# Kernel tuning notes

Measured on AMD Instinct MI355X. Metric: run time of the kernel, lower is better.

Reference implementation:

```python
import jax, jax.numpy as jnp
import numpy as np

EPS = 1e-5
N_HEADS = 4
N_GROUPS = 32


def group_norm(x, gamma, beta, num_groups):
    # x: (B, C, H, W)
    B, C, H, W = x.shape
    xg = x.reshape(B, num_groups, (C // num_groups) * H * W)
    mean = xg.mean(axis=2, keepdims=True)
    var = xg.var(axis=2, keepdims=True)
    xn = ((xg - mean) * jax.lax.rsqrt(var + EPS)).reshape(B, C, H, W)
    return xn * gamma[None, :, None, None] + beta[None, :, None, None]


def conv1x1(x, W, b=None):
    # 1x1 conv == channel-mixing matmul: (O,C) x (B,C,H,W) -> (B,O,H,W)
    y = jnp.einsum('oc,bchw->bohw', W, x)
    if b is not None:
        y = y + b[None, :, None, None]
    return y


def setup_inputs() -> dict:
    key = jax.random.key(0)
    ks = jax.random.split(key, 8)
    B, Cq, Cc, H, W = 2, 128, 128, 64, 64
    x = jax.random.normal(ks[0], (B, Cq, H, W), dtype=jnp.float32)
    context = jax.random.normal(ks[1], (B, Cc, H, W), dtype=jnp.float32)
    sq = Cq ** -0.5
    sc = Cc ** -0.5
    return {
        'x': x,
        'context': context,
        'gq': jnp.ones((Cq,), jnp.float32),
        'bq': jnp.zeros((Cq,), jnp.float32),
        'gctx': jnp.ones((Cc,), jnp.float32),
        'bctx': jnp.zeros((Cc,), jnp.float32),
        'Wq': jax.random.normal(ks[2], (Cq, Cq), jnp.float32) * sq,
        'Wk': jax.random.normal(ks[3], (Cq, Cc), jnp.float32) * sc,
        'Wv': jax.random.normal(ks[4], (Cq, Cc), jnp.float32) * sc,
        'Wout': jax.random.normal(ks[5], (Cq, Cq), jnp.float32) * 0.02,
        'bout': jnp.zeros((Cq,), jnp.float32),
        'alpha': jnp.asarray(1.0, jnp.float32),
    }


def reference(x, context, gq, bq, gctx, bctx, Wq, Wk, Wv, Wout, bout, alpha):
    B, C, H, W = x.shape
    hd = C // N_HEADS
    # QKV projections (GroupNorm + 1x1 conv); note v uses raw context (no norm)
    q = conv1x1(group_norm(x, gq, bq, N_GROUPS), Wq)
    k = conv1x1(group_norm(context, gctx, bctx, N_GROUPS), Wk)
    v = conv1x1(context, Wv)
    q = q.reshape(B, N_HEADS, hd, H * W)
    k = k.reshape(B, N_HEADS, hd, H * W)
    v = v.reshape(B, N_HEADS, hd, H * W)
    scale = jnp.asarray(hd ** 0.5, x.dtype)
    attn = jnp.einsum('bncd,bnce->bnde', q, k) / scale  # (B, nH, HW, HW)
    attn = jax.nn.softmax(attn, axis=-1)
    out = jnp.einsum('bnde,bnce->bncd', attn, v).reshape(B, C, H, W)
    return x + alpha * conv1x1(out, Wout, bout)
```

## Files before the change

kernel.cpp:

```cpp
#include <hip/hip_runtime.h>
#include <hip/hip_bf16.h>
#include <math.h>

#define L 4096
#define C 128
#define NH 4
#define HD 32
#define KS 4
#define EPSV 1e-5f

typedef short bf16x8 __attribute__((ext_vector_type(8)));
typedef float f32x4 __attribute__((ext_vector_type(4)));

static __device__ __forceinline__ unsigned pack2bf(float a, float b) {
    __hip_bfloat162 h = __float22bfloat162_rn(make_float2(a, b));
    unsigned u; __builtin_memcpy(&u, &h, 4); return u;
}
static __device__ __forceinline__ float bf_lo(unsigned u) {
    unsigned v = u << 16; float f; __builtin_memcpy(&f, &v, 4); return f;
}
static __device__ __forceinline__ float bf_hi(unsigned u) {
    unsigned v = u & 0xffff0000u; float f; __builtin_memcpy(&f, &v, 4); return f;
}
static __device__ __forceinline__ float fast_exp2(float x) {
    float t = fmaf(x, 8388608.f, 1064992212.f);
    int i = (int)t;
    float r; __builtin_memcpy(&r, &i, 4);
    return r;
}

__global__ __launch_bounds__(256) void gn_stats_kernel(
    const float* __restrict__ x, const float* __restrict__ ctx,
    float* __restrict__ stats)
{
    int bid = blockIdx.x;
    int t = threadIdx.x;
    const float* in = (bid < 256) ? x : ctx;
    int idx = bid & 255;
    const float4* p = (const float4*)(in + (size_t)(idx >> 2) * 16384
                                         + (size_t)(idx & 3) * 4096);
    float s = 0.f, s2 = 0.f;
    #pragma unroll
    for (int rr = 0; rr < 4; rr++) {
        float4 v = p[t + rr * 256];
        s  += v.x + v.y + v.z + v.w;
        s2 += v.x*v.x + v.y*v.y + v.z*v.z + v.w*v.w;
    }
    #pragma unroll
    for (int m = 32; m >= 1; m >>= 1) {
        s  += __shfl_xor(s, m);
        s2 += __shfl_xor(s2, m);
    }
    __shared__ float wsum[4][2];
    int w = t >> 6;
    if ((t & 63) == 0) { wsum[w][0] = s; wsum[w][1] = s2; }
    __syncthreads();
    if (t == 0) {
        float S  = wsum[0][0] + wsum[1][0] + wsum[2][0] + wsum[3][0];
        float S2 = wsum[0][1] + wsum[1][1] + wsum[2][1] + wsum[3][1];
        stats[bid * 2]     = S;
        stats[bid * 2 + 1] = S2;
    }
}

__global__ __launch_bounds__(256) void proj_kernel(
    const float* __restrict__ x, const float* __restrict__ ctx,
    const float* __restrict__ gq, const float* __restrict__ bq,
    const float* __restrict__ gctx, const float* __restrict__ bctx,
    const float* __restrict__ stats,
    const float* __restrict__ Wq, const float* __restrict__ Wk,
    const float* __restrict__ Wv,
    unsigned short* __restrict__ Qt, unsigned short* __restrict__ Kt,
    unsigned short* __restrict__ Vsw)
{
    int t = threadIdx.x;
    int w = t >> 6, lane = t & 63, n16 = lane & 15, quad = lane >> 4;
    int dtile = blockIdx.x * 32;
    int b = blockIdx.y, z = blockIdx.z;

    const float* in; const float* Wm; const float* gamma; const float* beta;
    int sel = 1, donorm = 1; float oscale = 1.f;
    if (z == 0)      { in = x;   Wm = Wq; gamma = gq;   beta = bq;   sel = 0;
                       oscale = 0.17677669529663689f * 1.4426950408889634f; }
    else if (z == 1) { in = ctx; Wm = Wk; gamma = gctx; beta = bctx; }
    else             { in = ctx; Wm = Wv; gamma = 0;    beta = 0;    donorm = 0; }

    __shared__ __attribute__((aligned(16))) unsigned short Xs[32 * 136];

    {
        int c0 = (t >> 3) * 4, d4 = (t & 7) * 4;
        const float* inb = in + (size_t)b * (C * L);
        float sc0 = 1.f, sh0 = 0.f;
        float scg[4], shg[4];
        if (donorm) {
            int gl = (sel * 256 + (b * 32 + (c0 >> 2)) * 4) * 2;
            float S  = stats[gl] + stats[gl + 2] + stats[gl + 4] + stats[gl + 6];
            float S2 = stats[gl + 1] + stats[gl + 3] + stats[gl + 5] + stats[gl + 7];
            float mean = S * (1.f / 16384.f);
            float var  = S2 * (1.f / 16384.f) - mean * mean;
            float inv  = rsqrtf(var + EPSV);
            #pragma unroll
            for (int j = 0; j < 4; j++) {
                scg[j] = inv * gamma[c0 + j];
                shg[j] = beta[c0 + j] - mean * scg[j];
            }
        } else {
            #pragma unroll
            for (int j = 0; j < 4; j++) { scg[j] = 1.f; shg[j] = 0.f; }
        }
        (void)sc0; (void)sh0;
        float vv[4][4];
        #pragma unroll
        for (int j = 0; j < 4; j++) {
            float4 v = *(const float4*)(inb + (size_t)(c0 + j) * L + dtile + d4);
            vv[j][0] = v.x * scg[j] + shg[j]; vv[j][1] = v.y * scg[j] + shg[j];
            vv[j][2] = v.z * scg[j] + shg[j]; vv[j][3] = v.w * scg[j] + shg[j];
        }
        #pragma unroll
        for (int i = 0; i < 4; i++) {
            uint2 pk;
            pk.x = pack2bf(vv[0][i], vv[1][i]);
            pk.y = pack2bf(vv[2][i], vv[3][i]);
            *(uint2*)&Xs[(d4 + i) * 136 + c0] = pk;
        }
    }

    bf16x8 wa[2][4];
    #pragma unroll
    for (int os2 = 0; os2 < 2; os2++) {
        const float* wr = Wm + (size_t)(((w + os2 * 4) * 16) + n16) * C + quad * 8;
        #pragma unroll
        for (int kk = 0; kk < 4; kk++) {
            float4 a  = *(const float4*)(wr + kk * 32);
            float4 b2 = *(const float4*)(wr + kk * 32 + 4);
            unsigned u4[4] = { pack2bf(a.x, a.y),  pack2bf(a.z, a.w),
                               pack2bf(b2.x, b2.y), pack2bf(b2.z, b2.w) };
            __builtin_memcpy(&wa[os2][kk], u4, 16);
        }
    }
    __syncthreads();

    f32x4 zero = {0.f, 0.f, 0.f, 0.f};
    f32x4 acc[2][2];
    acc[0][0] = zero; acc[0][1] = zero; acc[1][0] = zero; acc[1][1] = zero;
    #pragma unroll
    for (int kk = 0; kk < 4; kk++) {
        #pragma unroll
        for (int dg = 0; dg < 2; dg++) {
            bf16x8 xb;
            uint4 u = *(const uint4*)&Xs[(dg * 16 + n16) * 136 + kk * 32 + quad * 8];
            __builtin_memcpy(&xb, &u, 16);
            acc[0][dg] = __builtin_amdgcn_mfma_f32_16x16x32_bf16(wa[0][kk], xb, acc[0][dg], 0, 0, 0);
            acc[1][dg] = __builtin_amdgcn_mfma_f32_16x16x32_bf16(wa[1][kk], xb, acc[1][dg], 0, 0, 0);
        }
    }

    #pragma unroll
    for (int os2 = 0; os2 < 2; os2++) {
        int o = ((w + os2 * 4) * 16) + quad * 4;
        int h = o >> 5, c32 = o & 31;
        #pragma unroll
        for (int dg = 0; dg < 2; dg++) {
            int d = dtile + dg * 16 + n16;
            if (z < 2) {
                unsigned short* outp = (z == 0) ? Qt : Kt;
                uint2 pk;
                pk.x = pack2bf(acc[os2][dg][0] * oscale, acc[os2][dg][1] * oscale);
                pk.y = pack2bf(acc[os2][dg][2] * oscale, acc[os2][dg][3] * oscale);
                *(uint2*)(outp + ((size_t)(b * NH + h) * L + d) * HD + c32) = pk;
            } else {
                unsigned short* vb = Vsw + (size_t)(b * NH + h) * (L * HD)
                                   + (size_t)(d >> 3) * 256 + (d & 7);
                #pragma unroll
                for (int r = 0; r < 4; r++) {
                    __hip_bfloat16 hv = __float2bfloat16(acc[os2][dg][r]);
                    unsigned short us; __builtin_memcpy(&us, &hv, 2);
                    vb[(c32 + r) * 8] = us;
                }
            }
        }
    }
}

__global__ __launch_bounds__(256, 4) void flash_kernel(
    const unsigned short* __restrict__ Qt, const unsigned short* __restrict__ Kt,
    const unsigned short* __restrict__ Vsw, unsigned short* __restrict__ Po,
    float* __restrict__ Pl)
{
    __shared__ __attribute__((aligned(16))) unsigned short Ps[4 * 2 * 1152];

    int t = threadIdx.x;
    int w = t >> 6, lane = t & 63;
    int n16 = lane & 15, quad = lane >> 4;
    int bh = blockIdx.x;
    int qbase = blockIdx.y * 128 + w * 32;
    int ks = blockIdx.z;
    size_t hb = (size_t)bh * (L * HD);

    bf16x8 qf[2];
    #pragma unroll
    for (int sp = 0; sp < 2; sp++) {
        uint4 u = *(const uint4*)(Qt + hb + (size_t)(qbase + sp * 16 + n16) * HD + quad * 8);
        __builtin_memcpy(&qf[sp], &u, 16);
    }

    bf16x8 onesf;
    #pragma unroll
    for (int j = 0; j < 8; j++) onesf[j] = (short)0x3F80;

    const unsigned short* kfp = Kt + hb + (size_t)n16 * HD + quad * 8;
    const unsigned short* vfp = Vsw + hb + quad * 256 + n16 * 8;

    int e0 = ks * (L / KS);

    bf16x8 ka[2][4], va[2][4];
    #pragma unroll
    for (int et = 0; et < 4; et++) {
        uint4 u = *(const uint4*)(kfp + (size_t)(e0 + et * 16) * HD);
        __builtin_memcpy(&ka[0][et], &u, 16);
    }
    #pragma unroll
    for (int es = 0; es < 2; es++)
        #pragma unroll
        for (int f = 0; f < 2; f++) {
            uint4 u = *(const uint4*)(vfp + (size_t)(e0 + es * 32) * 32 + f * 128);
            __builtin_memcpy(&va[0][es * 2 + f], &u, 16);
        }

    f32x4 zero = {0.f, 0.f, 0.f, 0.f};
    f32x4 oacc[2][2], lacc[2];
    oacc[0][0] = zero; oacc[0][1] = zero; oacc[1][0] = zero; oacc[1][1] = zero;
    lacc[0] = zero; lacc[1] = zero;

    #pragma unroll 2
    for (int kt = 0; kt < L / KS / 64; kt++) {
        int cur = kt & 1, nxt = cur ^ 1;
        int enxt = e0 + (kt + 1) * 64;
        #pragma unroll
        for (int et = 0; et < 4; et++) {
            uint4 u = *(const uint4*)(kfp + (size_t)(enxt + et * 16) * HD);
            __builtin_memcpy(&ka[nxt][et], &u, 16);
        }
        #pragma unroll
        for (int es = 0; es < 2; es++)
            #pragma unroll
            for (int f = 0; f < 2; f++) {
                uint4 u = *(const uint4*)(vfp + (size_t)(enxt + es * 32) * 32 + f * 128);
                __builtin_memcpy(&va[nxt][es * 2 + f], &u, 16);
            }

        #pragma unroll
        for (int sp = 0; sp < 2; sp++) {
            f32x4 s[4];
            #pragma unroll
            for (int et = 0; et < 4; et++)
                s[et] = __builtin_amdgcn_mfma_f32_16x16x32_bf16(ka[cur][et], qf[sp], zero, 0, 0, 0);
            unsigned short* pw = Ps + ((w * 2 + sp) * 1152) + n16 * 72;
            #pragma unroll
            for (int et = 0; et < 4; et++) {
                uint2 pk;
                pk.x = pack2bf(fast_exp2(s[et][0]), fast_exp2(s[et][1]));
                pk.y = pack2bf(fast_exp2(s[et][2]), fast_exp2(s[et][3]));
                *(uint2*)(pw + et * 16 + quad * 4) = pk;
            }
        }

        #pragma unroll
        for (int sp = 0; sp < 2; sp++) {
            unsigned short* pw = Ps + ((w * 2 + sp) * 1152) + n16 * 72;
            #pragma unroll
            for (int es = 0; es < 2; es++) {
                bf16x8 pf;
                uint4 u = *(const uint4*)(pw + es * 32 + quad * 8);
                __builtin_memcpy(&pf, &u, 16);
                oacc[sp][0] = __builtin_amdgcn_mfma_f32_16x16x32_bf16(va[cur][es * 2 + 0], pf, oacc[sp][0], 0, 0, 0);
                oacc[sp][1] = __builtin_amdgcn_mfma_f32_16x16x32_bf16(va[cur][es * 2 + 1], pf, oacc[sp][1], 0, 0, 0);
                lacc[sp]    = __builtin_amdgcn_mfma_f32_16x16x32_bf16(onesf, pf, lacc[sp], 0, 0, 0);
            }
        }
    }

    #pragma unroll
    for (int sp = 0; sp < 2; sp++) {
        int dq = qbase + sp * 16 + n16;
        unsigned short* po = Po + ((size_t)(bh * KS + ks) * L + dq) * 32;
        uint2 pk0, pk1;
        pk0.x = pack2bf(oacc[sp][0][0], oacc[sp][0][1]);
        pk0.y = pack2bf(oacc[sp][0][2], oacc[sp][0][3]);
        pk1.x = pack2bf(oacc[sp][1][0], oacc[sp][1][1]);
        pk1.y = pack2bf(oacc[sp][1][2], oacc[sp][1][3]);
        *(uint2*)(po + quad * 4)      = pk0;
        *(uint2*)(po + 16 + quad * 4) = pk1;
        if (quad == 0)
            Pl[(size_t)(bh * KS + ks) * L + dq] = lacc[sp][0];
    }
}

__global__ __launch_bounds__(256) void final_kernel(
    const unsigned short* __restrict__ Po, const float* __restrict__ Pl,
    const float* __restrict__ x, const float* __restrict__ Wout,
    const float* __restrict__ bout, const float* __restrict__ alpha,
    float* __restrict__ out)
{
    int t = threadIdx.x;
    int w = t >> 6, lane = t & 63, n16 = lane & 15, quad = lane >> 4;
    int dtile = blockIdx.x * 16;
    int b = blockIdx.y;

    __shared__ __attribute__((aligned(16))) float Ot[128 * 20];
    unsigned short* Xs = (unsigned short*)Ot;

    {
        int d_l = t >> 4, c0 = (t & 15) * 8;
        int dq = dtile + d_l;
        int bh = b * NH + (c0 >> 5);
        int c32 = c0 & 31;
        float l = 0.f;
        float o8[8] = {0.f, 0.f, 0.f, 0.f, 0.f, 0.f, 0.f, 0.f};
        #pragma unroll
        for (int ks = 0; ks < KS; ks++) {
            size_t base = (size_t)(bh * KS + ks) * L + dq;
            l += Pl[base];
            uint4 u = *(const uint4*)(Po + base * 32 + c32);
            o8[0] += bf_lo(u.x); o8[1] += bf_hi(u.x);
            o8[2] += bf_lo(u.y); o8[3] += bf_hi(u.y);
            o8[4] += bf_lo(u.z); o8[5] += bf_hi(u.z);
            o8[6] += bf_lo(u.w); o8[7] += bf_hi(u.w);
        }
        float rl = 1.f / l;
        uint4 pk;
        pk.x = pack2bf(o8[0] * rl, o8[1] * rl);
        pk.y = pack2bf(o8[2] * rl, o8[3] * rl);
        pk.z = pack2bf(o8[4] * rl, o8[5] * rl);
        pk.w = pack2bf(o8[6] * rl, o8[7] * rl);
        *(uint4*)&Xs[d_l * 136 + c0] = pk;
    }

    bf16x8 wa[2][4];
    #pragma unroll
    for (int os2 = 0; os2 < 2; os2++) {
        const float* wr = Wout + (size_t)(((w + os2 * 4) * 16) + n16) * C + quad * 8;
        #pragma unroll
        for (int kk = 0; kk < 4; kk++) {
            float4 a  = *(const float4*)(wr + kk * 32);
            float4 b2 = *(const float4*)(wr + kk * 32 + 4);
            unsigned u4[4] = { pack2bf(a.x, a.y),  pack2bf(a.z, a.w),
                               pack2bf(b2.x, b2.y), pack2bf(b2.z, b2.w) };
            __builtin_memcpy(&wa[os2][kk], u4, 16);
        }
    }
    __syncthreads();

    f32x4 zero = {0.f, 0.f, 0.f, 0.f};
    f32x4 acc[2];
    acc[0] = zero; acc[1] = zero;
    #pragma unroll
    for (int kk = 0; kk < 4; kk++) {
        bf16x8 xb;
        uint4 u = *(const uint4*)&Xs[n16 * 136 + kk * 32 + quad * 8];
        __builtin_memcpy(&xb, &u, 16);
        acc[0] = __builtin_amdgcn_mfma_f32_16x16x32_bf16(wa[0][kk], xb, acc[0], 0, 0, 0);
        acc[1] = __builtin_amdgcn_mfma_f32_16x16x32_bf16(wa[1][kk], xb, acc[1], 0, 0, 0);
    }
    __syncthreads();

    #pragma unroll
    for (int os2 = 0; os2 < 2; os2++) {
        int o = ((w + os2 * 4) * 16) + quad * 4;
        #pragma unroll
        for (int r = 0; r < 4; r++)
            Ot[(o + r) * 20 + n16] = acc[os2][r];
    }
    __syncthreads();

    float al = alpha[0];
    int o = t >> 1, dh = (t & 1) * 8;
    float bo = bout[o];
    const float* xb2 = x + ((size_t)b * C + o) * L + dtile + dh;
    float* ob = out + ((size_t)b * C + o) * L + dtile + dh;
    #pragma unroll
    for (int jj = 0; jj < 2; jj++) {
        float4 a  = *(const float4*)&Ot[o * 20 + dh + jj * 4];
        float4 xv = *(const float4*)(xb2 + jj * 4);
        float4 r;
        r.x = xv.x + al * (a.x + bo);
        r.y = xv.y + al * (a.y + bo);
        r.z = xv.z + al * (a.z + bo);
        r.w = xv.w + al * (a.w + bo);
        *(float4*)(ob + jj * 4) = r;
    }
}

extern "C" void kernel_launch(void* const* d_in, const int* in_sizes, int n_in,
                              void* d_out, int out_size, void* d_ws, size_t ws_size,
                              hipStream_t stream) {
    const float* x     = (const float*)d_in[0];
    const float* ctx   = (const float*)d_in[1];
    const float* gq    = (const float*)d_in[2];
    const float* bq    = (const float*)d_in[3];
    const float* gctx  = (const float*)d_in[4];
    const float* bctx  = (const float*)d_in[5];
    const float* Wq    = (const float*)d_in[6];
    const float* Wk    = (const float*)d_in[7];
    const float* Wv    = (const float*)d_in[8];
    const float* Wout  = (const float*)d_in[9];
    const float* bout  = (const float*)d_in[10];
    const float* alpha = (const float*)d_in[11];
    float* out = (float*)d_out;

    char* ws = (char*)d_ws;
    unsigned short* Qt  = (unsigned short*)(ws);
    unsigned short* Kt  = (unsigned short*)(ws + 2097152);
    unsigned short* Vsw = (unsigned short*)(ws + 4194304);
    unsigned short* Po  = (unsigned short*)(ws + 6291456);
    float*          Pl  = (float*)(ws + 14680064);
    float*          stats = (float*)(ws + 15204352);

    gn_stats_kernel<<<512, 256, 0, stream>>>(x, ctx, stats);
    proj_kernel<<<dim3(128, 2, 3), 256, 0, stream>>>(x, ctx, gq, bq, gctx, bctx,
                                                     stats, Wq, Wk, Wv, Qt, Kt, Vsw);
    flash_kernel<<<dim3(8, 32, KS), 256, 0, stream>>>(Qt, Kt, Vsw, Po, Pl);
    final_kernel<<<dim3(256, 2), 256, 0, stream>>>(Po, Pl, x, Wout, bout, alpha, out);
}
```

Baseline: 127.8 us.

## Keep softmax probabilities in registers via f16 MFMA, removing the LDS round-trip

The flash kernel no longer writes exp'd scores to shared memory and reads them back for the PV product. The S accumulator layout from the 16x16x32 MFMA is fed directly as the B operand of 16x16x16 f16 MFMAs. This needs V re-laid out in f16 with a 4-wide swizzle, written by the projection kernel. The cost is twice as many PV/row-sum MFMAs at half depth, V loads that are no longer double-buffered across iterations, and f16 range for V and P, with round-toward-zero packing of P.

Result: slower. 134.0 us (+4.9%).

```diff
diff --git a/kernel.cpp b/kernel.cpp
--- a/kernel.cpp
+++ b/kernel.cpp
@@ -11,6 +11,7 @@
 
 typedef short bf16x8 __attribute__((ext_vector_type(8)));
 typedef float f32x4 __attribute__((ext_vector_type(4)));
+typedef _Float16 f16x4 __attribute__((ext_vector_type(4)));
 
 static __device__ __forceinline__ unsigned pack2bf(float a, float b) {
     __hip_bfloat162 h = __float22bfloat162_rn(make_float2(a, b));
@@ -90,7 +91,6 @@
     {
         int c0 = (t >> 3) * 4, d4 = (t & 7) * 4;
         const float* inb = in + (size_t)b * (C * L);
-        float sc0 = 1.f, sh0 = 0.f;
         float scg[4], shg[4];
         if (donorm) {
             int gl = (sel * 256 + (b * 32 + (c0 >> 2)) * 4) * 2;
@@ -108,7 +108,6 @@
             #pragma unroll
             for (int j = 0; j < 4; j++) { scg[j] = 1.f; shg[j] = 0.f; }
         }
-        (void)sc0; (void)sh0;
         float vv[4][4];
         #pragma unroll
         for (int j = 0; j < 4; j++) {
@@ -170,12 +169,12 @@
                 *(uint2*)(outp + ((size_t)(b * NH + h) * L + d) * HD + c32) = pk;
             } else {
                 unsigned short* vb = Vsw + (size_t)(b * NH + h) * (L * HD)
-                                   + (size_t)(d >> 3) * 256 + (d & 7);
+                                   + ((size_t)(d >> 2) * 32 + c32) * 4 + (d & 3);
                 #pragma unroll
                 for (int r = 0; r < 4; r++) {
-                    __hip_bfloat16 hv = __float2bfloat16(acc[os2][dg][r]);
+                    _Float16 hv = (_Float16)acc[os2][dg][r];
                     unsigned short us; __builtin_memcpy(&us, &hv, 2);
-                    vb[(c32 + r) * 8] = us;
+                    vb[r * 4] = us;
                 }
             }
         }
@@ -187,8 +186,6 @@
     const unsigned short* __restrict__ Vsw, unsigned short* __restrict__ Po,
     float* __restrict__ Pl)
 {
-    __shared__ __attribute__((aligned(16))) unsigned short Ps[4 * 2 * 1152];
-
     int t = threadIdx.x;
     int w = t >> 6, lane = t & 63;
     int n16 = lane & 15, quad = lane >> 4;
@@ -204,28 +201,21 @@
         __builtin_memcpy(&qf[sp], &u, 16);
     }
 
-    bf16x8 onesf;
-    #pragma unroll
-    for (int j = 0; j < 8; j++) onesf[j] = (short)0x3F80;
+    f16x4 onesf;
+    #pragma unroll
+    for (int j = 0; j < 4; j++) onesf[j] = (_Float16)1.0f;
 
     const unsigned short* kfp = Kt + hb + (size_t)n16 * HD + quad * 8;
-    const unsigned short* vfp = Vsw + hb + quad * 256 + n16 * 8;
+    const unsigned short* vfp = Vsw + hb + quad * 128 + n16 * 4;
 
     int e0 = ks * (L / KS);
 
-    bf16x8 ka[2][4], va[2][4];
+    bf16x8 ka[2][4];
     #pragma unroll
     for (int et = 0; et < 4; et++) {
         uint4 u = *(const uint4*)(kfp + (size_t)(e0 + et * 16) * HD);
         __builtin_memcpy(&ka[0][et], &u, 16);
     }
-    #pragma unroll
-    for (int es = 0; es < 2; es++)
-        #pragma unroll
-        for (int f = 0; f < 2; f++) {
-            uint4 u = *(const uint4*)(vfp + (size_t)(e0 + es * 32) * 32 + f * 128);
-            __builtin_memcpy(&va[0][es * 2 + f], &u, 16);
-        }
 
     f32x4 zero = {0.f, 0.f, 0.f, 0.f};
     f32x4 oacc[2][2], lacc[2];
@@ -241,13 +231,17 @@
             uint4 u = *(const uint4*)(kfp + (size_t)(enxt + et * 16) * HD);
             __builtin_memcpy(&ka[nxt][et], &u, 16);
         }
-        #pragma unroll
-        for (int es = 0; es < 2; es++)
-            #pragma unroll
-            for (int f = 0; f < 2; f++) {
-                uint4 u = *(const uint4*)(vfp + (size_t)(enxt + es * 32) * 32 + f * 128);
-                __builtin_memcpy(&va[nxt][es * 2 + f], &u, 16);
-            }
+        f16x4 va[4][2];
+        {
+            const unsigned short* vt = vfp + (size_t)(e0 + kt * 64) * 32;
+            #pragma unroll
+            for (int et = 0; et < 4; et++)
+                #pragma unroll
+                for (int ch = 0; ch < 2; ch++) {
+                    uint2 u = *(const uint2*)(vt + et * 512 + ch * 64);
+                    __builtin_memcpy(&va[et][ch], &u, 8);
+                }
+        }
 
         #pragma unroll
         for (int sp = 0; sp < 2; sp++) {
@@ -255,27 +249,19 @@
             #pragma unroll
             for (int et = 0; et < 4; et++)
                 s[et] = __builtin_amdgcn_mfma_f32_16x16x32_bf16(ka[cur][et], qf[sp], zero, 0, 0, 0);
-            unsigned short* pw = Ps + ((w * 2 + sp) * 1152) + n16 * 72;
+            f16x4 pf[4];
             #pragma unroll
             for (int et = 0; et < 4; et++) {
-                uint2 pk;
-                pk.x = pack2bf(fast_exp2(s[et][0]), fast_exp2(s[et][1]));
-                pk.y = pack2bf(fast_exp2(s[et][2]), fast_exp2(s[et][3]));
-                *(uint2*)(pw + et * 16 + quad * 4) = pk;
+                auto lo = __builtin_amdgcn_cvt_pkrtz(fast_exp2(s[et][0]), fast_exp2(s[et][1]));
+                auto hi = __builtin_amdgcn_cvt_pkrtz(fast_exp2(s[et][2]), fast_exp2(s[et][3]));
+                pf[et][0] = (_Float16)lo[0]; pf[et][1] = (_Float16)lo[1];
+                pf[et][2] = (_Float16)hi[0]; pf[et][3] = (_Float16)hi[1];
             }
-        }
-
-        #pragma unroll
-        for (int sp = 0; sp < 2; sp++) {
-            unsigned short* pw = Ps + ((w * 2 + sp) * 1152) + n16 * 72;
-            #pragma unroll
-            for (int es = 0; es < 2; es++) {
-                bf16x8 pf;
-                uint4 u = *(const uint4*)(pw + es * 32 + quad * 8);
-                __builtin_memcpy(&pf, &u, 16);
-                oacc[sp][0] = __builtin_amdgcn_mfma_f32_16x16x32_bf16(va[cur][es * 2 + 0], pf, oacc[sp][0], 0, 0, 0);
-                oacc[sp][1] = __builtin_amdgcn_mfma_f32_16x16x32_bf16(va[cur][es * 2 + 1], pf, oacc[sp][1], 0, 0, 0);
-                lacc[sp]    = __builtin_amdgcn_mfma_f32_16x16x32_bf16(onesf, pf, lacc[sp], 0, 0, 0);
+            #pragma unroll
+            for (int et = 0; et < 4; et++) {
+                oacc[sp][0] = __builtin_amdgcn_mfma_f32_16x16x16f16(va[et][0], pf[et], oacc[sp][0], 0, 0, 0);
+                oacc[sp][1] = __builtin_amdgcn_mfma_f32_16x16x16f16(va[et][1], pf[et], oacc[sp][1], 0, 0, 0);
+                lacc[sp]    = __builtin_amdgcn_mfma_f32_16x16x16f16(onesf,     pf[et], lacc[sp],    0, 0, 0);
             }
         }
     }
```
